# Performance work log

Hardware: AMD Instinct MI355X
Metric: run time of the kernel (lower is better)

Reference implementation:

```python
import jax, jax.numpy as jnp
import numpy as np

N_NODES = 200000
N_GRAPHS = 4000


def _sage_conv(x, src, dst, W_l, b_l, W_r, num_nodes):
    # PyG SAGEConv (aggr='mean'): out = lin_l(mean_{j in N(i)} x_j) + lin_r(x_i)
    msg_sum = jax.ops.segment_sum(x[src], dst, num_segments=num_nodes)      # [N, d]
    deg = jax.ops.segment_sum(jnp.ones_like(src, dtype=x.dtype), dst,
                              num_segments=num_nodes)                       # [N]
    mean_nbr = msg_sum / jnp.maximum(deg, 1.0)[:, None]
    return mean_nbr @ W_l.T + b_l + x @ W_r.T


def setup_inputs() -> dict:
    key = jax.random.key(0)
    ks = jax.random.split(key, 10)
    in_ch, hid, out = 32, 64, 2
    E = 3200000
    x = jax.random.normal(ks[0], (N_NODES, in_ch), dtype=jnp.float32)
    edge_index = jax.random.randint(ks[1], (2, E), 0, N_NODES, dtype=jnp.int64)
    batch = jnp.sort(jax.random.randint(ks[2], (N_NODES,), 0, N_GRAPHS, dtype=jnp.int64))

    def glorot(k, shape):
        lim = 1.0 / np.sqrt(shape[1])
        return jax.random.uniform(k, shape, jnp.float32, -lim, lim)

    return {
        "x": x,
        "edge_index": edge_index,
        "batch": batch,
        "W1_l": glorot(ks[3], (hid, in_ch)),
        "b1": jnp.zeros((hid,), jnp.float32),
        "W1_r": glorot(ks[4], (hid, in_ch)),
        "W2_l": glorot(ks[5], (hid, hid)),
        "b2": jnp.zeros((hid,), jnp.float32),
        "W2_r": glorot(ks[6], (hid, hid)),
        "W_lin": glorot(ks[7], (out, hid)),
        "b_lin": jnp.zeros((out,), jnp.float32),
    }


def reference(x, edge_index, batch, W1_l, b1, W1_r, W2_l, b2, W2_r, W_lin, b_lin):
    src, dst = edge_index[0], edge_index[1]
    h = jax.nn.relu(_sage_conv(x, src, dst, W1_l, b1, W1_r, N_NODES))
    h = jax.nn.relu(_sage_conv(h, src, dst, W2_l, b2, W2_r, N_NODES))
    # global_mean_pool over graph ids
    pool_sum = jax.ops.segment_sum(h, batch, num_segments=N_GRAPHS)          # [G, 64]
    cnt = jax.ops.segment_sum(jnp.ones_like(batch, dtype=h.dtype), batch,
                              num_segments=N_GRAPHS)                          # [G]
    pooled = pool_sum / jnp.maximum(cnt, 1.0)[:, None]
    return pooled @ W_lin.T + b_lin
```

## Files before the change

### kernel.cpp

```cpp
#include <hip/hip_runtime.h>
#include <hip/hip_bf16.h>


#define WS_ALIGN 64
#define EPB 4096
#define BSHIFT 8
#define BNODES 256
#define BCAP 6144
#define MAXNB 1024

typedef short bf16x8 __attribute__((ext_vector_type(8)));
typedef float f32x4 __attribute__((ext_vector_type(4)));

__device__ inline unsigned short f2bf(float f) {
    unsigned u = __float_as_uint(f);
    return (unsigned short)((u + 0x7fffu + ((u >> 16) & 1u)) >> 16);
}

__device__ inline void acc8(const uint4 u, float* a) {
    a[0] += __uint_as_float(u.x << 16);
    a[1] += __uint_as_float(u.x & 0xffff0000u);
    a[2] += __uint_as_float(u.y << 16);
    a[3] += __uint_as_float(u.y & 0xffff0000u);
    a[4] += __uint_as_float(u.z << 16);
    a[5] += __uint_as_float(u.z & 0xffff0000u);
    a[6] += __uint_as_float(u.w << 16);
    a[7] += __uint_as_float(u.w & 0xffff0000u);
}


__global__ void prep_kernel(const float* __restrict__ x, unsigned short* __restrict__ xb,
                            const float* __restrict__ W1_l, const float* __restrict__ W1_r,
                            const float* __restrict__ W2_l, const float* __restrict__ W2_r,
                            unsigned short* __restrict__ whi1, unsigned short* __restrict__ whi2,
                            int* __restrict__ bucketCursor, float* __restrict__ pool,
                            int N, int NB, int G, int total4) {
    const int gid = blockIdx.x * blockDim.x + threadIdx.x;
    if (gid < total4) {
        const float4 v = reinterpret_cast<const float4*>(x)[gid];
        ushort4 o;
        o.x = f2bf(v.x); o.y = f2bf(v.y); o.z = f2bf(v.z); o.w = f2bf(v.w);
        reinterpret_cast<ushort4*>(xb)[gid] = o;
    }
    if (gid < NB) bucketCursor[gid] = gid * BCAP;
    if (gid < G * 64) pool[gid] = 0.0f;
    if (gid < 64 * 64) {
        const int o = gid >> 6, k = gid & 63;
        const float v = (k < 32) ? W1_l[o * 32 + k] : W1_r[o * 32 + (k - 32)];
        whi1[gid] = f2bf(v);
    }
    if (gid < 64 * 128) {
        const int o = gid >> 7, k = gid & 127;
        const float v = (k < 64) ? W2_l[o * 64 + k] : W2_r[o * 64 + (k - 64)];
        whi2[gid] = f2bf(v);
    }
}


__global__ __launch_bounds__(256) void bucket_scatter_kernel(const int* __restrict__ src,
                                                             const int* __restrict__ dst,
                                                             int* __restrict__ bucketCursor,
                                                             unsigned* __restrict__ bucketData,
                                                             int E, int NB) {
    __shared__ int hist[MAXNB];
    __shared__ int cur[MAXNB];
    const int t = threadIdx.x;
    for (int i = t; i < MAXNB; i += 256) hist[i] = 0;
    __syncthreads();
    const int eBase = blockIdx.x * EPB + t;
    int s[16], b[16], dl[16];
#pragma unroll
    for (int j = 0; j < 16; ++j) {
        int e = eBase + j * 256;
        if (e < E) {
            int d = dst[e];
            s[j]  = src[e];
            b[j]  = d >> BSHIFT;
            dl[j] = d & (BNODES - 1);
            atomicAdd(&hist[b[j]], 1);
        } else {
            b[j] = -1;
        }
    }
    __syncthreads();
    for (int bb = t; bb < NB; bb += 256)
        if (hist[bb] > 0) cur[bb] = atomicAdd(&bucketCursor[bb], hist[bb]);
    __syncthreads();
#pragma unroll
    for (int j = 0; j < 16; ++j) {
        if (b[j] >= 0) {
            int pos = atomicAdd(&cur[b[j]], 1);
            if (pos < (b[j] + 1) * BCAP)
                bucketData[pos] = ((unsigned)s[j] << BSHIFT) | (unsigned)dl[j];
        }
    }
}

__global__ __launch_bounds__(256) void csr_build_kernel(const unsigned* __restrict__ bucketData,
                                                        const int* __restrict__ bucketCursor,
                                                        int* __restrict__ offs,
                                                        int* __restrict__ offe,
                                                        int* __restrict__ csr_src,
                                                        int N) {
    __shared__ int cnt[BNODES];
    __shared__ int sscan[BNODES];
    __shared__ int cur[BNODES];
    const int t   = threadIdx.x;
    const int bkt = blockIdx.x;
    const int nodeBase = bkt << BSHIFT;
    const int regionBase = bkt * BCAP;
    const int count = min(bucketCursor[bkt] - regionBase, BCAP);
    cnt[t] = 0;
    __syncthreads();
    for (int k = regionBase + t; k < regionBase + count; k += 256)
        atomicAdd(&cnt[bucketData[k] & (BNODES - 1)], 1);
    __syncthreads();
    int v0 = cnt[t];
    sscan[t] = v0;
    __syncthreads();
    for (int off = 1; off < 256; off <<= 1) {
        int v = (t >= off) ? sscan[t - off] : 0;
        __syncthreads();
        sscan[t] += v;
        __syncthreads();
    }
    const int excl = sscan[t] - v0;
    cur[t] = excl;
    const int node = nodeBase + t;
    if (node < N) {
        offs[node] = regionBase + excl;
        offe[node] = regionBase + excl + v0;
    }
    __syncthreads();
    for (int k = regionBase + t; k < regionBase + count; k += 256) {
        const unsigned v = bucketData[k];
        const int d = (int)(v & (BNODES - 1));
        const int pos = regionBase + atomicAdd(&cur[d], 1);
        csr_src[pos] = (int)(v >> BSHIFT);
    }
}


template <int DIN, bool POOL>
__launch_bounds__(256)
__global__ void fused_agg_mfma_kernel(const unsigned short* __restrict__ featb,
                                      const unsigned short* __restrict__ whi,
                                      const float* __restrict__ bias,
                                      const int* __restrict__ csr_src,
                                      const int* __restrict__ offs,
                                      const int* __restrict__ offe,
                                      unsigned short* __restrict__ houtb,
                                      const int* __restrict__ batch,
                                      float* __restrict__ pool_sum,
                                      int N, int nSteps) {
    constexpr int K     = 2 * DIN;
    constexpr int STR   = K + 8;
    constexpr int D8    = DIN / 8;
    constexpr int NPN   = 256 / D8;
    constexpr int NPASS = 64 / NPN;
    __shared__ unsigned short A_s[64 * STR];
    __shared__ float poolLds[POOL ? 64 * 65 : 1];
    const int tid = threadIdx.x;
    const int nodeBase = blockIdx.x * 64;

    if (POOL) {
        for (int i = tid; i < 64 * 65; i += 256) poolLds[i] = 0.0f;
    }

    for (int i = tid; i < 64 * D8; i += 256) {
        const int node = i / D8, q = i % D8;
        const int n = min(nodeBase + node, N - 1);
        const uint4 u = *reinterpret_cast<const uint4*>(featb + (size_t)n * DIN + q * 8);
        *reinterpret_cast<uint4*>(&A_s[node * STR + DIN + q * 8]) = u;
    }

    {
        const int part = tid % D8;
        const uint4* base = reinterpret_cast<const uint4*>(featb);
#pragma unroll
        for (int pass = 0; pass < NPASS; ++pass) {
            const int node = pass * NPN + tid / D8;
            const int n = nodeBase + node;
            unsigned short* dp = &A_s[node * STR + part * 8];
            if (n < N) {
                const int beg = offs[n];
                const int end = offe[n];
                float a[8] = {0.f, 0.f, 0.f, 0.f, 0.f, 0.f, 0.f, 0.f};
                int k = beg;
                for (; k + 8 <= end; k += 8) {
                    int s[8];
#pragma unroll
                    for (int j = 0; j < 8; ++j) s[j] = csr_src[k + j];
                    uint4 u[8];
#pragma unroll
                    for (int j = 0; j < 8; ++j) u[j] = base[(size_t)s[j] * D8 + part];
#pragma unroll
                    for (int j = 0; j < 8; ++j) acc8(u[j], a);
                }
                for (; k + 4 <= end; k += 4) {
                    const int s0 = csr_src[k + 0];
                    const int s1 = csr_src[k + 1];
                    const int s2 = csr_src[k + 2];
                    const int s3 = csr_src[k + 3];
                    const uint4 u0 = base[(size_t)s0 * D8 + part];
                    const uint4 u1 = base[(size_t)s1 * D8 + part];
                    const uint4 u2 = base[(size_t)s2 * D8 + part];
                    const uint4 u3 = base[(size_t)s3 * D8 + part];
                    acc8(u0, a); acc8(u1, a); acc8(u2, a); acc8(u3, a);
                }
                for (; k < end; ++k) {
                    const uint4 u = base[(size_t)csr_src[k] * D8 + part];
                    acc8(u, a);
                }
                const float inv = 1.0f / fmaxf((float)(end - beg), 1.0f);
                ushort4 lo4, hi4;
                lo4.x = f2bf(a[0] * inv); lo4.y = f2bf(a[1] * inv);
                lo4.z = f2bf(a[2] * inv); lo4.w = f2bf(a[3] * inv);
                hi4.x = f2bf(a[4] * inv); hi4.y = f2bf(a[5] * inv);
                hi4.z = f2bf(a[6] * inv); hi4.w = f2bf(a[7] * inv);
                *reinterpret_cast<ushort4*>(dp)     = lo4;
                *reinterpret_cast<ushort4*>(dp + 4) = hi4;
            } else {
                const ushort4 z = {0, 0, 0, 0};
                *reinterpret_cast<ushort4*>(dp)     = z;
                *reinterpret_cast<ushort4*>(dp + 4) = z;
            }
        }
    }
    __syncthreads();

    const int lane = tid & 63;
    const int wave = tid >> 6;
    const int lr = lane & 15;
    const int q  = lane >> 4;
    f32x4 acc[4];
#pragma unroll
    for (int t = 0; t < 4; ++t) {
        const float b = bias[t * 16 + lr];
        acc[t] = (f32x4){b, b, b, b};
    }
    const unsigned short* Arow = &A_s[(wave * 16 + lr) * STR + q * 8];
    const unsigned short* Brow = whi + (size_t)lr * K + q * 8;
    for (int s = 0; s < nSteps; ++s) {
        const bf16x8 af = *reinterpret_cast<const bf16x8*>(Arow + s * 32);
#pragma unroll
        for (int t = 0; t < 4; ++t) {
            const bf16x8 bh = *reinterpret_cast<const bf16x8*>(
                Brow + (size_t)t * 16 * K + s * 32);
            acc[t] = __builtin_amdgcn_mfma_f32_16x16x32_bf16(af, bh, acc[t], 0, 0, 0);
        }
    }

    if (POOL) {
        const int g0 = batch[nodeBase];
        float ag[4] = {0.f, 0.f, 0.f, 0.f};
        int gcur = -1;
        for (int reg = 0; reg < 4; ++reg) {
            const int n = nodeBase + wave * 16 + q * 4 + reg;
            if (n >= N) break;
            const int g = batch[n];
            if (g != gcur) {
                if (gcur >= 0) {
#pragma unroll
                    for (int t = 0; t < 4; ++t)
                        atomicAdd(&poolLds[(gcur - g0) * 65 + t * 16 + lr], ag[t]);
                }
                gcur = g;
                ag[0] = ag[1] = ag[2] = ag[3] = 0.f;
            }
#pragma unroll
            for (int t = 0; t < 4; ++t)
                ag[t] += fmaxf(acc[t][reg], 0.0f);
        }
        if (gcur >= 0) {
#pragma unroll
            for (int t = 0; t < 4; ++t)
                atomicAdd(&poolLds[(gcur - g0) * 65 + t * 16 + lr], ag[t]);
        }
        __syncthreads();
        const int glast = batch[min(nodeBase + 63, N - 1)];
        const int S = glast - g0 + 1;
        for (int i = tid; i < S * 64; i += 256) {
            const int r = i >> 6, c = i & 63;
            const float v = poolLds[r * 65 + c];
            float* dstp = &pool_sum[(size_t)(g0 + r) * 64 + c];
            if (r == 0 || r == S - 1) atomicAdd(dstp, v);
            else *dstp = v;
        }
    } else {
        for (int reg = 0; reg < 4; ++reg) {
            const int n = nodeBase + wave * 16 + q * 4 + reg;
            if (n >= N) break;
#pragma unroll
            for (int t = 0; t < 4; ++t)
                houtb[(size_t)n * 64 + t * 16 + lr] = f2bf(fmaxf(acc[t][reg], 0.0f));
        }
    }
}


__device__ inline int lower_bound_batch(const int* __restrict__ batch, int N, int key) {
    int lo = 0, hi = N;
    while (lo < hi) {
        const int mid = (lo + hi) >> 1;
        if (batch[mid] < key) lo = mid + 1; else hi = mid;
    }
    return lo;
}

__global__ void final_kernel(const float* __restrict__ pool_sum,
                             const int* __restrict__ batch,
                             const float* __restrict__ W_lin,
                             const float* __restrict__ b_lin,
                             float* __restrict__ out, int G, int N) {
    int t = blockIdx.x * blockDim.x + threadIdx.x;
    if (t >= G * 2) return;
    int g = t >> 1, o = t & 1;
    const int c0 = lower_bound_batch(batch, N, g);
    const int c1 = lower_bound_batch(batch, N, g + 1);
    float inv = 1.0f / fmaxf((float)(c1 - c0), 1.0f);
    float acc = b_lin[o];
#pragma unroll
    for (int c = 0; c < 64; ++c)
        acc = fmaf(pool_sum[(size_t)g * 64 + c] * inv, W_lin[o * 64 + c], acc);
    out[t] = acc;
}

extern "C" void kernel_launch(void* const* d_in, const int* in_sizes, int n_in,
                              void* d_out, int out_size, void* d_ws, size_t ws_size,
                              hipStream_t stream) {
    const float* x     = (const float*)d_in[0];
    const int*   ei    = (const int*)d_in[1];
    const int*   batch = (const int*)d_in[2];
    const float* W1_l  = (const float*)d_in[3];
    const float* b1    = (const float*)d_in[4];
    const float* W1_r  = (const float*)d_in[5];
    const float* W2_l  = (const float*)d_in[6];
    const float* b2    = (const float*)d_in[7];
    const float* W2_r  = (const float*)d_in[8];
    const float* W_lin = (const float*)d_in[9];
    const float* b_lin = (const float*)d_in[10];

    const int N = in_sizes[0] / 32;
    const int E = in_sizes[1] / 2;
    const int G = out_size / 2;
    const int* src = ei;
    const int* dst = ei + E;
    const int NB = (N + BNODES - 1) >> BSHIFT;

    char* p = (char*)d_ws;
    auto carve = [&](size_t bytes) -> void* {
        void* r = (void*)p;
        p += (bytes + (WS_ALIGN - 1)) / WS_ALIGN * WS_ALIGN;
        return r;
    };
    int*            bucketCursor = (int*)carve((size_t)MAXNB * 4);
    unsigned*       bucketData   = (unsigned*)carve((size_t)NB * BCAP * 4);
    int*            offs         = (int*)carve((size_t)N * 4);
    int*            offe         = (int*)carve((size_t)N * 4);
    int*            csr_src      = (int*)carve((size_t)NB * BCAP * 4);
    unsigned short* xb           = (unsigned short*)carve((size_t)N * 32 * 2);
    unsigned short* h1b          = (unsigned short*)carve((size_t)N * 64 * 2);
    unsigned short* whi1         = (unsigned short*)carve(64 * 64 * 2);
    unsigned short* whi2         = (unsigned short*)carve(64 * 128 * 2);
    float*          pool         = (float*)carve((size_t)G * 64 * 4);
    float*          out          = (float*)d_out;

    const int TB = 256;
    const int total4 = N * 32 / 4;
    prep_kernel<<<(total4 + TB - 1) / TB, TB, 0, stream>>>(
        x, xb, W1_l, W1_r, W2_l, W2_r, whi1, whi2, bucketCursor, pool,
        N, NB, G, total4);
    bucket_scatter_kernel<<<(E + EPB - 1) / EPB, TB, 0, stream>>>(src, dst, bucketCursor,
                                                                  bucketData, E, NB);
    csr_build_kernel<<<NB, TB, 0, stream>>>(bucketData, bucketCursor, offs, offe, csr_src, N);

    fused_agg_mfma_kernel<32, false><<<(N + 63) / 64, TB, 0, stream>>>(
        xb, whi1, b1, csr_src, offs, offe, h1b, nullptr, nullptr, N, 2);

    fused_agg_mfma_kernel<64, true><<<(N + 63) / 64, TB, 0, stream>>>(
        h1b, whi2, b2, csr_src, offs, offe, nullptr, batch, pool, N, 4);

    final_kernel<<<(G * 2 + TB - 1) / TB, TB, 0, stream>>>(pool, batch, W_lin, b_lin,
                                                           out, G, N);
}
```

Measured before the change: 344.6 us.

## Split layer-2 aggregation from MFMA into separate gather and dense kernels

Layer 2 previously gathered neighbours and ran the MFMA in one fused kernel. It is now split into a standalone per-node gather/mean kernel that writes a bf16 aggregate buffer, followed by a dense MFMA kernel with pooling. The standalone gather has no LDS or barrier constraints, so it can keep more loads in flight and reach higher occupancy. The cost is an extra N×64 bf16 write and read plus one more kernel launch. The fused kernel keeps only the non-pool path for layer 1.

After: 361.9 us. +5.0%, slower.

```diff
diff --git a/kernel.cpp b/kernel.cpp
--- a/kernel.cpp
+++ b/kernel.cpp
@@ -137,6 +137,161 @@
         const int d = (int)(v & (BNODES - 1));
         const int pos = regionBase + atomicAdd(&cur[d], 1);
         csr_src[pos] = (int)(v >> BSHIFT);
+    }
+}
+
+
+template <int D>
+__global__ void agg_bf16_kernel(const unsigned short* __restrict__ featb,
+                                const int* __restrict__ csr_src,
+                                const int* __restrict__ offs,
+                                const int* __restrict__ offe,
+                                unsigned short* __restrict__ aggb, int N) {
+    constexpr int TPN = D / 8;
+    int tid  = blockIdx.x * blockDim.x + threadIdx.x;
+    int node = tid / TPN;
+    int part = tid % TPN;
+    if (node >= N) return;
+    const int beg = offs[node];
+    const int end = offe[node];
+    const uint4* base = reinterpret_cast<const uint4*>(featb);
+    float a[8] = {0.f, 0.f, 0.f, 0.f, 0.f, 0.f, 0.f, 0.f};
+    int k = beg;
+    for (; k + 8 <= end; k += 8) {
+        int s[8];
+#pragma unroll
+        for (int j = 0; j < 8; ++j) s[j] = csr_src[k + j];
+        uint4 u[8];
+#pragma unroll
+        for (int j = 0; j < 8; ++j) u[j] = base[(size_t)s[j] * TPN + part];
+#pragma unroll
+        for (int j = 0; j < 8; ++j) acc8(u[j], a);
+    }
+    for (; k + 4 <= end; k += 4) {
+        const int s0 = csr_src[k + 0];
+        const int s1 = csr_src[k + 1];
+        const int s2 = csr_src[k + 2];
+        const int s3 = csr_src[k + 3];
+        const uint4 u0 = base[(size_t)s0 * TPN + part];
+        const uint4 u1 = base[(size_t)s1 * TPN + part];
+        const uint4 u2 = base[(size_t)s2 * TPN + part];
+        const uint4 u3 = base[(size_t)s3 * TPN + part];
+        acc8(u0, a); acc8(u1, a); acc8(u2, a); acc8(u3, a);
+    }
+    for (; k < end; ++k) {
+        const uint4 u = base[(size_t)csr_src[k] * TPN + part];
+        acc8(u, a);
+    }
+    const float inv = 1.0f / fmaxf((float)(end - beg), 1.0f);
+    ushort4 lo, hi;
+    lo.x = f2bf(a[0] * inv); lo.y = f2bf(a[1] * inv);
+    lo.z = f2bf(a[2] * inv); lo.w = f2bf(a[3] * inv);
+    hi.x = f2bf(a[4] * inv); hi.y = f2bf(a[5] * inv);
+    hi.z = f2bf(a[6] * inv); hi.w = f2bf(a[7] * inv);
+    unsigned short* dstp = aggb + (size_t)node * D + part * 8;
+    *reinterpret_cast<ushort4*>(dstp)     = lo;
+    *reinterpret_cast<ushort4*>(dstp + 4) = hi;
+}
+
+
+template <int DIN, bool POOL>
+__launch_bounds__(256)
+__global__ void mfma_dense_kernel(const unsigned short* __restrict__ aggb,
+                                  const unsigned short* __restrict__ xinb,
+                                  const unsigned short* __restrict__ whi,
+                                  const float* __restrict__ bias,
+                                  unsigned short* __restrict__ houtb,
+                                  const int* __restrict__ batch,
+                                  float* __restrict__ pool_sum,
+                                  int N, int nSteps) {
+    constexpr int K   = 2 * DIN;
+    constexpr int STR = K + 8;
+    constexpr int D8  = DIN / 8;
+    __shared__ unsigned short A_s[64 * STR];
+    __shared__ float poolLds[POOL ? 64 * 65 : 1];
+    const int tid = threadIdx.x;
+    const int nodeBase = blockIdx.x * 64;
+
+    if (POOL) {
+        for (int i = tid; i < 64 * 65; i += 256) poolLds[i] = 0.0f;
+    }
+    for (int i = tid; i < 64 * D8 * 2; i += 256) {
+        const int half = i / (64 * D8);
+        const int j = i % (64 * D8);
+        const int node = j / D8, q = j % D8;
+        const int n = min(nodeBase + node, N - 1);
+        const unsigned short* srcp = half ? xinb : aggb;
+        const uint4 u = *reinterpret_cast<const uint4*>(srcp + (size_t)n * DIN + q * 8);
+        *reinterpret_cast<uint4*>(&A_s[node * STR + half * DIN + q * 8]) = u;
+    }
+    __syncthreads();
+
+    const int lane = tid & 63;
+    const int wave = tid >> 6;
+    const int lr = lane & 15;
+    const int q  = lane >> 4;
+    f32x4 acc[4];
+#pragma unroll
+    for (int t = 0; t < 4; ++t) {
+        const float b = bias[t * 16 + lr];
+        acc[t] = (f32x4){b, b, b, b};
+    }
+    const unsigned short* Arow = &A_s[(wave * 16 + lr) * STR + q * 8];
+    const unsigned short* Brow = whi + (size_t)lr * K + q * 8;
+    for (int s = 0; s < nSteps; ++s) {
+        const bf16x8 af = *reinterpret_cast<const bf16x8*>(Arow + s * 32);
+#pragma unroll
+        for (int t = 0; t < 4; ++t) {
+            const bf16x8 bh = *reinterpret_cast<const bf16x8*>(
+                Brow + (size_t)t * 16 * K + s * 32);
+            acc[t] = __builtin_amdgcn_mfma_f32_16x16x32_bf16(af, bh, acc[t], 0, 0, 0);
+        }
+    }
+
+    if (POOL) {
+        const int g0 = batch[nodeBase];
+        float ag[4] = {0.f, 0.f, 0.f, 0.f};
+        int gcur = -1;
+        for (int reg = 0; reg < 4; ++reg) {
+            const int n = nodeBase + wave * 16 + q * 4 + reg;
+            if (n >= N) break;
+            const int g = batch[n];
+            if (g != gcur) {
+                if (gcur >= 0) {
+#pragma unroll
+                    for (int t = 0; t < 4; ++t)
+                        atomicAdd(&poolLds[(gcur - g0) * 65 + t * 16 + lr], ag[t]);
+                }
+                gcur = g;
+                ag[0] = ag[1] = ag[2] = ag[3] = 0.f;
+            }
+#pragma unroll
+            for (int t = 0; t < 4; ++t)
+                ag[t] += fmaxf(acc[t][reg], 0.0f);
+        }
+        if (gcur >= 0) {
+#pragma unroll
+            for (int t = 0; t < 4; ++t)
+                atomicAdd(&poolLds[(gcur - g0) * 65 + t * 16 + lr], ag[t]);
+        }
+        __syncthreads();
+        const int glast = batch[min(nodeBase + 63, N - 1)];
+        const int S = glast - g0 + 1;
+        for (int i = tid; i < S * 64; i += 256) {
+            const int r = i >> 6, c = i & 63;
+            const float v = poolLds[r * 65 + c];
+            float* dstp = &pool_sum[(size_t)(g0 + r) * 64 + c];
+            if (r == 0 || r == S - 1) atomicAdd(dstp, v);
+            else *dstp = v;
+        }
+    } else {
+        for (int reg = 0; reg < 4; ++reg) {
+            const int n = nodeBase + wave * 16 + q * 4 + reg;
+            if (n >= N) break;
+#pragma unroll
+            for (int t = 0; t < 4; ++t)
+                houtb[(size_t)n * 64 + t * 16 + lr] = f2bf(fmaxf(acc[t][reg], 0.0f));
+        }
     }
 }
 
@@ -159,13 +314,8 @@
     constexpr int NPN   = 256 / D8;
     constexpr int NPASS = 64 / NPN;
     __shared__ unsigned short A_s[64 * STR];
-    __shared__ float poolLds[POOL ? 64 * 65 : 1];
     const int tid = threadIdx.x;
     const int nodeBase = blockIdx.x * 64;
-
-    if (POOL) {
-        for (int i = tid; i < 64 * 65; i += 256) poolLds[i] = 0.0f;
-    }
 
     for (int i = tid; i < 64 * D8; i += 256) {
         const int node = i / D8, q = i % D8;
@@ -251,50 +401,12 @@
         }
     }
 
-    if (POOL) {
-        const int g0 = batch[nodeBase];
-        float ag[4] = {0.f, 0.f, 0.f, 0.f};
-        int gcur = -1;
-        for (int reg = 0; reg < 4; ++reg) {
-            const int n = nodeBase + wave * 16 + q * 4 + reg;
-            if (n >= N) break;
-            const int g = batch[n];
-            if (g != gcur) {
-                if (gcur >= 0) {
-#pragma unroll
-                    for (int t = 0; t < 4; ++t)
-                        atomicAdd(&poolLds[(gcur - g0) * 65 + t * 16 + lr], ag[t]);
-                }
-                gcur = g;
-                ag[0] = ag[1] = ag[2] = ag[3] = 0.f;
-            }
-#pragma unroll
-            for (int t = 0; t < 4; ++t)
-                ag[t] += fmaxf(acc[t][reg], 0.0f);
-        }
-        if (gcur >= 0) {
-#pragma unroll
-            for (int t = 0; t < 4; ++t)
-                atomicAdd(&poolLds[(gcur - g0) * 65 + t * 16 + lr], ag[t]);
-        }
-        __syncthreads();
-        const int glast = batch[min(nodeBase + 63, N - 1)];
-        const int S = glast - g0 + 1;
-        for (int i = tid; i < S * 64; i += 256) {
-            const int r = i >> 6, c = i & 63;
-            const float v = poolLds[r * 65 + c];
-            float* dstp = &pool_sum[(size_t)(g0 + r) * 64 + c];
-            if (r == 0 || r == S - 1) atomicAdd(dstp, v);
-            else *dstp = v;
-        }
-    } else {
-        for (int reg = 0; reg < 4; ++reg) {
-            const int n = nodeBase + wave * 16 + q * 4 + reg;
-            if (n >= N) break;
-#pragma unroll
-            for (int t = 0; t < 4; ++t)
-                houtb[(size_t)n * 64 + t * 16 + lr] = f2bf(fmaxf(acc[t][reg], 0.0f));
-        }
+    for (int reg = 0; reg < 4; ++reg) {
+        const int n = nodeBase + wave * 16 + q * 4 + reg;
+        if (n >= N) break;
+#pragma unroll
+        for (int t = 0; t < 4; ++t)
+            houtb[(size_t)n * 64 + t * 16 + lr] = f2bf(fmaxf(acc[t][reg], 0.0f));
     }
 }
 
@@ -360,6 +472,7 @@
     int*            offe         = (int*)carve((size_t)N * 4);
     int*            csr_src      = (int*)carve((size_t)NB * BCAP * 4);
     unsigned short* xb           = (unsigned short*)carve((size_t)N * 32 * 2);
+    unsigned short* aggb         = (unsigned short*)carve((size_t)N * 64 * 2);
     unsigned short* h1b          = (unsigned short*)carve((size_t)N * 64 * 2);
     unsigned short* whi1         = (unsigned short*)carve(64 * 64 * 2);
     unsigned short* whi2         = (unsigned short*)carve(64 * 128 * 2);
@@ -378,8 +491,10 @@
     fused_agg_mfma_kernel<32, false><<<(N + 63) / 64, TB, 0, stream>>>(
         xb, whi1, b1, csr_src, offs, offe, h1b, nullptr, nullptr, N, 2);
 
-    fused_agg_mfma_kernel<64, true><<<(N + 63) / 64, TB, 0, stream>>>(
-        h1b, whi2, b2, csr_src, offs, offe, nullptr, batch, pool, N, 4);
+    agg_bf16_kernel<64><<<((size_t)N * 8 + TB - 1) / TB, TB, 0, stream>>>(
+        h1b, csr_src, offs, offe, aggb, N);
+    mfma_dense_kernel<64, true><<<(N + 63) / 64, TB, 0, stream>>>(
+        aggb, h1b, whi2, b2, nullptr, batch, pool, N, 4);
 
     final_kernel<<<(G * 2 + TB - 1) / TB, TB, 0, stream>>>(pool, batch, W_lin, b_lin,
                                                            out, G, N);
```

## Give each wave its own 16 rows and drop the block barrier

Applied to the files above, without the earlier changes.

Each wavefront now gathers and averages neighbour features only for the 16 rows it later feeds into its own MFMA tile. That lets the block-wide __syncthreads between gather and matmul be replaced by a wave-local LDS wait, so waves no longer stall on the slowest high-degree node in the block. The pool LDS buffer shrinks from 64 to 16 graph rows, which cuts shared-memory use and may raise occupancy; runs beyond the 16th graph fall back to global atomics. The cost is a small extra barrier after zeroing the pool buffer and possible extra global atomics in rare wide-span blocks.

Measured after the change: 337.0 us. 2.2% less time.

```diff
diff --git a/kernel.cpp b/kernel.cpp
--- a/kernel.cpp
+++ b/kernel.cpp
@@ -156,32 +156,36 @@
     constexpr int K     = 2 * DIN;
     constexpr int STR   = K + 8;
     constexpr int D8    = DIN / 8;
-    constexpr int NPN   = 256 / D8;
-    constexpr int NPASS = 64 / NPN;
+    constexpr int NPW   = 64 / D8;
+    constexpr int NPASS = 16 / NPW;
     __shared__ unsigned short A_s[64 * STR];
-    __shared__ float poolLds[POOL ? 64 * 65 : 1];
-    const int tid = threadIdx.x;
+    __shared__ float poolLds[POOL ? 16 * 65 : 1];
+    const int tid  = threadIdx.x;
+    const int lane = tid & 63;
+    const int wave = tid >> 6;
     const int nodeBase = blockIdx.x * 64;
+    const int rowBase  = wave * 16;
 
     if (POOL) {
-        for (int i = tid; i < 64 * 65; i += 256) poolLds[i] = 0.0f;
-    }
-
-    for (int i = tid; i < 64 * D8; i += 256) {
-        const int node = i / D8, q = i % D8;
-        const int n = min(nodeBase + node, N - 1);
+        for (int i = tid; i < 16 * 65; i += 256) poolLds[i] = 0.0f;
+        __syncthreads();
+    }
+
+    for (int i = lane; i < 16 * D8; i += 64) {
+        const int row = rowBase + i / D8, q = i % D8;
+        const int n = min(nodeBase + row, N - 1);
         const uint4 u = *reinterpret_cast<const uint4*>(featb + (size_t)n * DIN + q * 8);
-        *reinterpret_cast<uint4*>(&A_s[node * STR + DIN + q * 8]) = u;
+        *reinterpret_cast<uint4*>(&A_s[row * STR + DIN + q * 8]) = u;
     }
 
     {
-        const int part = tid % D8;
+        const int part = lane % D8;
         const uint4* base = reinterpret_cast<const uint4*>(featb);
 #pragma unroll
         for (int pass = 0; pass < NPASS; ++pass) {
-            const int node = pass * NPN + tid / D8;
-            const int n = nodeBase + node;
-            unsigned short* dp = &A_s[node * STR + part * 8];
+            const int row = rowBase + pass * NPW + lane / D8;
+            const int n = nodeBase + row;
+            unsigned short* dp = &A_s[row * STR + part * 8];
             if (n < N) {
                 const int beg = offs[n];
                 const int end = offe[n];
@@ -227,10 +231,10 @@
             }
         }
     }
-    __syncthreads();
-
-    const int lane = tid & 63;
-    const int wave = tid >> 6;
+
+    asm volatile("s_waitcnt lgkmcnt(0)" ::: "memory");
+    __builtin_amdgcn_sched_barrier(0);
+
     const int lr = lane & 15;
     const int q  = lane >> 4;
     f32x4 acc[4];
@@ -239,7 +243,7 @@
         const float b = bias[t * 16 + lr];
         acc[t] = (f32x4){b, b, b, b};
     }
-    const unsigned short* Arow = &A_s[(wave * 16 + lr) * STR + q * 8];
+    const unsigned short* Arow = &A_s[(rowBase + lr) * STR + q * 8];
     const unsigned short* Brow = whi + (size_t)lr * K + q * 8;
     for (int s = 0; s < nSteps; ++s) {
         const bf16x8 af = *reinterpret_cast<const bf16x8*>(Arow + s * 32);
@@ -255,16 +259,24 @@
         const int g0 = batch[nodeBase];
         float ag[4] = {0.f, 0.f, 0.f, 0.f};
         int gcur = -1;
+        auto flush_run = [&](int g) {
+            const int r = g - g0;
+            if (r < 16) {
+#pragma unroll
+                for (int t = 0; t < 4; ++t)
+                    atomicAdd(&poolLds[r * 65 + t * 16 + lr], ag[t]);
+            } else {
+#pragma unroll
+                for (int t = 0; t < 4; ++t)
+                    atomicAdd(&pool_sum[(size_t)g * 64 + t * 16 + lr], ag[t]);
+            }
+        };
         for (int reg = 0; reg < 4; ++reg) {
-            const int n = nodeBase + wave * 16 + q * 4 + reg;
+            const int n = nodeBase + rowBase + q * 4 + reg;
             if (n >= N) break;
             const int g = batch[n];
             if (g != gcur) {
-                if (gcur >= 0) {
-#pragma unroll
-                    for (int t = 0; t < 4; ++t)
-                        atomicAdd(&poolLds[(gcur - g0) * 65 + t * 16 + lr], ag[t]);
-                }
+                if (gcur >= 0) flush_run(gcur);
                 gcur = g;
                 ag[0] = ag[1] = ag[2] = ag[3] = 0.f;
             }
@@ -272,14 +284,10 @@
             for (int t = 0; t < 4; ++t)
                 ag[t] += fmaxf(acc[t][reg], 0.0f);
         }
-        if (gcur >= 0) {
-#pragma unroll
-            for (int t = 0; t < 4; ++t)
-                atomicAdd(&poolLds[(gcur - g0) * 65 + t * 16 + lr], ag[t]);
-        }
+        if (gcur >= 0) flush_run(gcur);
         __syncthreads();
         const int glast = batch[min(nodeBase + 63, N - 1)];
-        const int S = glast - g0 + 1;
+        const int S = min(glast - g0 + 1, 16);
         for (int i = tid; i < S * 64; i += 256) {
             const int r = i >> 6, c = i & 63;
             const float v = poolLds[r * 65 + c];
@@ -289,7 +297,7 @@
         }
     } else {
         for (int reg = 0; reg < 4; ++reg) {
-            const int n = nodeBase + wave * 16 + q * 4 + reg;
+            const int n = nodeBase + rowBase + q * 4 + reg;
             if (n >= N) break;
 #pragma unroll
             for (int t = 0; t < 4; ++t)
```
